# Optimization experiments

Measured on AMD Instinct MI355X. Metric: run time of the kernel, lower is better.

The kernel has to match this reference:

```python
import jax, jax.numpy as jnp
import numpy as np

B, H, E = 1024, 2048, 1024

def _xavier(key, shape):
    # torch xavier_normal_ on [1, out, in]: std = sqrt(2/(fan_in+fan_out)) over last two dims
    fan_out, fan_in = shape[-2], shape[-1]
    std = (2.0 / (fan_in + fan_out)) ** 0.5
    return jax.random.normal(key, shape, jnp.float32) * std

def setup_inputs() -> dict:
    key = jax.random.key(0)
    ks = jax.random.split(key, 17)
    inp = {
        'x': jax.random.normal(ks[0], (B, E, 1), jnp.float32),
        'c': jax.random.normal(ks[1], (B, H, 1), jnp.float32),
        'h': jax.random.normal(ks[2], (B, H, 1), jnp.float32),
        'W_xi': _xavier(ks[3], (1, H, E)), 'W_hi': _xavier(ks[4], (1, H, H)), 'B_i': _xavier(ks[5], (1, H, 1)),
        'W_xg': _xavier(ks[6], (1, H, E)), 'W_hg': _xavier(ks[7], (1, H, H)), 'B_g': _xavier(ks[8], (1, H, 1)),
        'W_xf': _xavier(ks[9], (1, H, E)), 'W_hf': _xavier(ks[10], (1, H, H)), 'B_f': _xavier(ks[11], (1, H, 1)),
        'W_xo': _xavier(ks[12], (1, H, E)), 'W_ho': _xavier(ks[13], (1, H, H)), 'B_o': _xavier(ks[14], (1, H, 1)),
        'W_hy': _xavier(ks[15], (1, E, H)), 'B_y': _xavier(ks[16], (1, E, 1)),
    }
    return inp

def reference(x, c, h, W_xi, W_hi, B_i, W_xg, W_hg, B_g, W_xf, W_hf, B_f, W_xo, W_ho, B_o, W_hy, B_y):
    # jnp.matmul broadcasts the leading batch dim: [1,H,E] @ [B,E,1] -> [B,H,1]
    i = jax.nn.sigmoid(jnp.matmul(W_xi, x) + jnp.matmul(W_hi, h) + B_i)
    g = jnp.tanh(jnp.matmul(W_xg, x) + jnp.matmul(W_hg, h) + B_g)
    f = jax.nn.sigmoid(jnp.matmul(W_xf, x) + jnp.matmul(W_hf, h) + B_f)
    c_new = f * c + i * g
    o = jax.nn.sigmoid(jnp.matmul(W_xo, x) + jnp.matmul(W_ho, h) + B_o)
    h_new = o * c_new  # NOTE: source uses o*c (no tanh), faithful to original
    y = jnp.tanh(jnp.matmul(W_hy, h_new) + B_y)
    return (y, c_new, h_new)
```

## Files before the change

kernel.cpp:

```cpp
#include <hip/hip_runtime.h>

#define B_SZ 1024
#define H_SZ 2048
#define E_SZ 1024

typedef float  f32x4 __attribute__((ext_vector_type(4)));
typedef short  s16x8 __attribute__((ext_vector_type(8)));

__device__ __forceinline__ unsigned short f2bf(float f) {
    unsigned u = __float_as_uint(f);
    u = u + 0x7fffu + ((u >> 16) & 1u);
    return (unsigned short)(u >> 16);
}
__device__ __forceinline__ float bf2f(unsigned short s) {
    return __uint_as_float(((unsigned)s) << 16);
}
__device__ __forceinline__ float sigm(float v) {
    return 1.0f / (1.0f + __expf(-v));
}
__device__ __forceinline__ unsigned cvtpk(float lo, float hi) {
    unsigned r;
    asm("v_cvt_pk_bf16_f32 %0, %1, %2" : "=v"(r) : "v"(lo), "v"(hi));
    return r;
}

__device__ __forceinline__ void gll(const unsigned short* g, unsigned short* l) {
    __builtin_amdgcn_global_load_lds(
        (const __attribute__((address_space(1))) unsigned int*)g,
        (__attribute__((address_space(3))) unsigned int*)l, 16, 0, 0);
}

struct CastArgs {
    const float*    src[10];
    unsigned short* dst[10];
    int             n[10];
};

__global__ __launch_bounds__(256) void cast_kernel(CastArgs a) {
    const int arr = blockIdx.y;
    const int n = a.n[arr];
    const float* __restrict__ s = a.src[arr];
    unsigned short* __restrict__ d = a.dst[arr];
    const int stride = gridDim.x * 256 * 4;
    for (int i = (blockIdx.x * 256 + threadIdx.x) * 4; i < n; i += stride) {
        float4 v = *(const float4*)(s + i);
        ushort4 o;
        o.x = f2bf(v.x); o.y = f2bf(v.y); o.z = f2bf(v.z); o.w = f2bf(v.w);
        *(ushort4*)(d + i) = o;
    }
}

__device__ __forceinline__ void gemm_gates4(
    const unsigned short* __restrict__ A,
    const unsigned short* __restrict__ W0,
    const unsigned short* __restrict__ W1,
    const unsigned short* __restrict__ W2,
    const unsigned short* __restrict__ W3,
    int ld, int kLen, int m0, int n0h,
    unsigned short* lA, unsigned short* lB,
    f32x4 acc[4][4], int t)
{
    const int lane = t & 63;
    const int w    = t >> 6;
    const int wr   = (w >> 1) << 6;
    const int wc   = (w & 1) << 6;
    const int lr   = lane & 15;
    const int q4   = lane >> 4;

    const int srow = t >> 3;
    const int scol = ((t & 7) ^ (srow & 7)) << 3;
    const unsigned short* gA = A + (size_t)(m0 + srow) * ld + scol;
    const size_t st32 = (size_t)32 * ld;
    const size_t boff = (size_t)(n0h + srow) * ld + scol;
    const unsigned short* gB0 = W0 + boff;
    const unsigned short* gB1 = W1 + boff;
    const unsigned short* gB2 = W2 + boff;
    const unsigned short* gB3 = W3 + boff;

    const int cb0 = ((q4    ) ^ (lr & 7)) << 3;
    const int cb1 = ((4 + q4) ^ (lr & 7)) << 3;

    for (int k0 = 0; k0 < kLen; k0 += 64) {
#pragma unroll
        for (int p = 0; p < 4; ++p)
            gll(gA + k0 + p * st32, lA + (t + 256 * p) * 8);
        gll(gB0 + k0, lB + t * 8);
        gll(gB1 + k0, lB + (t + 256) * 8);
        gll(gB2 + k0, lB + (t + 512) * 8);
        gll(gB3 + k0, lB + (t + 768) * 8);
        __syncthreads();

#pragma unroll
        for (int ks = 0; ks < 2; ++ks) {
            const int cb = ks ? cb1 : cb0;
            s16x8 af[4], bfr[4];
#pragma unroll
            for (int i = 0; i < 4; ++i)
                af[i] = *(const s16x8*)(lA + (wr + i * 16 + lr) * 64 + cb);
#pragma unroll
            for (int j = 0; j < 4; ++j)
                bfr[j] = *(const s16x8*)(lB + (wc + j * 16 + lr) * 64 + cb);
#pragma unroll
            for (int i = 0; i < 4; ++i)
#pragma unroll
                for (int j = 0; j < 4; ++j)
                    acc[i][j] = __builtin_amdgcn_mfma_f32_16x16x32_bf16(
                        af[i], bfr[j], acc[i][j], 0, 0, 0);
        }
        __syncthreads();
    }
}

struct GatesCellArgs {
    const unsigned short *Xb, *Hb, *Wxb, *Whb;
    const float *bias[4];
    const float *cin;
    float *c_out, *h_out;
    unsigned short *HnB;
};

__global__ __launch_bounds__(256, 2) void gates_cell_kernel(GatesCellArgs a) {
    __shared__ unsigned short smem[16384];
    unsigned short* lA = smem;
    unsigned short* lB = smem + 8192;

    const int t   = threadIdx.x;
    const int b   = blockIdx.x;
    const int xcd = b & 7;
    const int i_  = b >> 3;
    const int nt  = xcd * 8 + (i_ >> 3);
    const int m0  = (i_ & 7) * 128;
    const int n0h = nt * 32;

    const size_t HE = (size_t)H_SZ * E_SZ, HH = (size_t)H_SZ * H_SZ;

    f32x4 acc[4][4] = {};
    gemm_gates4(a.Xb, a.Wxb, a.Wxb + HE, a.Wxb + 2 * HE, a.Wxb + 3 * HE,
                E_SZ, E_SZ, m0, n0h, lA, lB, acc, t);
    gemm_gates4(a.Hb, a.Whb, a.Whb + HH, a.Whb + 2 * HH, a.Whb + 3 * HH,
                H_SZ, H_SZ, m0, n0h, lA, lB, acc, t);

    const int lane = t & 63, w = t >> 6;
    const int wr = (w >> 1) << 6, wc = (w & 1) << 6;
    const int lr = lane & 15, rq = (lane >> 4) << 2;
#pragma unroll
    for (int j = 0; j < 4; ++j) {
        const int col = wc + j * 16 + lr;
        const int q   = col >> 5;
        const float bv = a.bias[q][n0h + (col & 31)];
#pragma unroll
        for (int i = 0; i < 4; ++i) {
#pragma unroll
            for (int r = 0; r < 4; ++r) {
                const int row = wr + i * 16 + rq + r;
                const float v = acc[i][j][r] + bv;
                const float act = (q == 1) ? tanhf(v) : sigm(v);
                smem[row * 128 + col] = f2bf(act);
            }
        }
    }
    __syncthreads();

    {
        const int row = t >> 1;
        const int hc  = (t & 1) * 16;
        const unsigned short* ex = smem + row * 128;
        s16x8 i0 = *(const s16x8*)(ex + hc);
        s16x8 i1 = *(const s16x8*)(ex + hc + 8);
        s16x8 g0 = *(const s16x8*)(ex + 32 + hc);
        s16x8 g1 = *(const s16x8*)(ex + 32 + hc + 8);
        s16x8 fg0 = *(const s16x8*)(ex + 64 + hc);
        s16x8 fg1 = *(const s16x8*)(ex + 64 + hc + 8);
        s16x8 o0 = *(const s16x8*)(ex + 96 + hc);
        s16x8 o1 = *(const s16x8*)(ex + 96 + hc + 8);

        const size_t gidx = (size_t)(m0 + row) * H_SZ + n0h + hc;
        float cn[16], hn[16];
#pragma unroll
        for (int k = 0; k < 16; ++k) {
            const float iv = bf2f((unsigned short)((k < 8 ? i0[k] : i1[k - 8])));
            const float gv = bf2f((unsigned short)((k < 8 ? g0[k] : g1[k - 8])));
            const float fv = bf2f((unsigned short)((k < 8 ? fg0[k] : fg1[k - 8])));
            const float ov = bf2f((unsigned short)((k < 8 ? o0[k] : o1[k - 8])));
            const float cv = a.cin[gidx + k];
            cn[k] = fv * cv + iv * gv;
            hn[k] = ov * cn[k];
        }
#pragma unroll
        for (int k = 0; k < 16; k += 4) {
            *(float4*)(a.c_out + gidx + k) = make_float4(cn[k], cn[k+1], cn[k+2], cn[k+3]);
            *(float4*)(a.h_out + gidx + k) = make_float4(hn[k], hn[k+1], hn[k+2], hn[k+3]);
            ushort4 hb;
            hb.x = f2bf(hn[k]);     hb.y = f2bf(hn[k+1]);
            hb.z = f2bf(hn[k+2]);   hb.w = f2bf(hn[k+3]);
            *(ushort4*)(a.HnB + gidx + k) = hb;
        }
    }
}

__device__ __forceinline__ void gemm_bk128(
    const unsigned short* __restrict__ A,
    const float* __restrict__ W,
    int ld, int kLen, int m0, int n0,
    unsigned short* lA, unsigned short* lB,
    f32x4 acc[4][4], int t)
{
    const int lane = t & 63;
    const int w    = t >> 6;
    const int wr   = (w >> 1) << 6;
    const int wc   = (w & 1) << 6;
    const int lr   = lane & 15;
    const int q4   = lane >> 4;

    const int srow = t >> 4;
    const int sblk = ((t & 15) ^ srow) << 3;
    const unsigned short* gA = A + (size_t)(m0 + srow) * ld + sblk;
    const float*          gW = W + (size_t)(n0 + srow) * ld + sblk;
    const size_t st16 = (size_t)16 * ld;

    f32x4 f0[8], f1[8];
#pragma unroll
    for (int p = 0; p < 8; ++p) {
        const float* s = gW + p * st16;
        f0[p] = *(const f32x4*)(s);
        f1[p] = *(const f32x4*)(s + 4);
    }

    for (int k0 = 0; k0 < kLen; k0 += 128) {
#pragma unroll
        for (int p = 0; p < 8; ++p) {
            uint4 pk;
            pk.x = cvtpk(f0[p].x, f0[p].y);
            pk.y = cvtpk(f0[p].z, f0[p].w);
            pk.z = cvtpk(f1[p].x, f1[p].y);
            pk.w = cvtpk(f1[p].z, f1[p].w);
            *(uint4*)(lB + (t + 256 * p) * 8) = pk;
        }
#pragma unroll
        for (int p = 0; p < 8; ++p)
            gll(gA + k0 + p * st16, lA + (t + 256 * p) * 8);
        __syncthreads();

        if (k0 + 128 < kLen) {
#pragma unroll
            for (int p = 0; p < 8; ++p) {
                const float* s = gW + (k0 + 128) + p * st16;
                f0[p] = *(const f32x4*)(s);
                f1[p] = *(const f32x4*)(s + 4);
            }
        }

#pragma unroll
        for (int ks = 0; ks < 4; ++ks) {
            s16x8 af[4], bfr[4];
#pragma unroll
            for (int i = 0; i < 4; ++i) {
                const int ra = wr + i * 16 + lr;
                af[i] = *(const s16x8*)(lA + ra * 128 +
                         ((((ks << 2) + q4) ^ (ra & 15)) << 3));
            }
#pragma unroll
            for (int j = 0; j < 4; ++j) {
                const int rb = wc + j * 16 + lr;
                bfr[j] = *(const s16x8*)(lB + rb * 128 +
                          ((((ks << 2) + q4) ^ (rb & 15)) << 3));
            }
#pragma unroll
            for (int i = 0; i < 4; ++i)
#pragma unroll
                for (int j = 0; j < 4; ++j)
                    acc[i][j] = __builtin_amdgcn_mfma_f32_16x16x32_bf16(
                        af[i], bfr[j], acc[i][j], 0, 0, 0);
        }
        __syncthreads();
    }
}

__global__ __launch_bounds__(256, 2) void y_split_kernel(
    const unsigned short* __restrict__ Hn,
    const float* __restrict__ Wy,
    float* __restrict__ part)
{
    __shared__ unsigned short lA[128 * 128];
    __shared__ unsigned short lB[128 * 128];
    const int t   = threadIdx.x;
    const int b   = blockIdx.x;
    const int xcd = b & 7;
    const int i_  = b >> 3;
    const int ns  = xcd * 4 + (i_ >> 3);
    const int m0  = (i_ & 7) * 128;
    const int n0  = (ns >> 2) * 128;
    const int s   = ns & 3;

    f32x4 acc[4][4] = {};
    gemm_bk128(Hn + s * 512, Wy + s * 512, H_SZ, 512, m0, n0, lA, lB, acc, t);

    const int lane = t & 63, w = t >> 6;
    const int wr = (w >> 1) << 6, wc = (w & 1) << 6;
    const int lr = lane & 15, rq = (lane >> 4) << 2;
    float* P = part + (size_t)s * B_SZ * E_SZ;
#pragma unroll
    for (int i = 0; i < 4; ++i) {
#pragma unroll
        for (int j = 0; j < 4; ++j) {
            const int n = n0 + wc + j * 16 + lr;
#pragma unroll
            for (int r = 0; r < 4; ++r) {
                const int m = m0 + wr + i * 16 + rq + r;
                P[(size_t)m * E_SZ + n] = acc[i][j][r];
            }
        }
    }
}

__global__ __launch_bounds__(256) void y_reduce_kernel(
    const float* __restrict__ part, const float* __restrict__ by,
    float* __restrict__ yout)
{
    const size_t BE = (size_t)B_SZ * E_SZ;
    const int idx = (blockIdx.x * 256 + threadIdx.x) * 4;
    float4 a = *(const float4*)(part + idx);
    float4 b2 = *(const float4*)(part + BE + idx);
    float4 c2 = *(const float4*)(part + 2 * BE + idx);
    float4 d2 = *(const float4*)(part + 3 * BE + idx);
    const int col = idx & (E_SZ - 1);
    float4 bv = *(const float4*)(by + col);
    float4 o;
    o.x = tanhf(a.x + b2.x + c2.x + d2.x + bv.x);
    o.y = tanhf(a.y + b2.y + c2.y + d2.y + bv.y);
    o.z = tanhf(a.z + b2.z + c2.z + d2.z + bv.z);
    o.w = tanhf(a.w + b2.w + c2.w + d2.w + bv.w);
    *(float4*)(yout + idx) = o;
}

extern "C" void kernel_launch(void* const* d_in, const int* in_sizes, int n_in,
                              void* d_out, int out_size, void* d_ws, size_t ws_size,
                              hipStream_t stream) {
    const float* x   = (const float*)d_in[0];
    const float* c   = (const float*)d_in[1];
    const float* h   = (const float*)d_in[2];
    const float* Wxi = (const float*)d_in[3];
    const float* Whi = (const float*)d_in[4];
    const float* Bi  = (const float*)d_in[5];
    const float* Wxg = (const float*)d_in[6];
    const float* Whg = (const float*)d_in[7];
    const float* Bg  = (const float*)d_in[8];
    const float* Wxf = (const float*)d_in[9];
    const float* Whf = (const float*)d_in[10];
    const float* Bf  = (const float*)d_in[11];
    const float* Wxo = (const float*)d_in[12];
    const float* Who = (const float*)d_in[13];
    const float* Bo  = (const float*)d_in[14];
    const float* Why = (const float*)d_in[15];
    const float* By  = (const float*)d_in[16];

    const size_t BE = (size_t)B_SZ * E_SZ, BH = (size_t)B_SZ * H_SZ;
    const size_t HE = (size_t)H_SZ * E_SZ, HH = (size_t)H_SZ * H_SZ;

    unsigned short* ws  = (unsigned short*)d_ws;
    unsigned short* Xb  = ws;
    unsigned short* Hb  = Xb + BE;
    unsigned short* Wxb = Hb + BH;
    unsigned short* Whb = Wxb + 4 * HE;
    unsigned short* HnB = Whb + 4 * HH;
    float*          ypart = (float*)(HnB + BH);

    CastArgs ca;
    ca.src[0] = x;   ca.dst[0] = Xb;          ca.n[0] = (int)BE;
    ca.src[1] = h;   ca.dst[1] = Hb;          ca.n[1] = (int)BH;
    ca.src[2] = Wxi; ca.dst[2] = Wxb;         ca.n[2] = (int)HE;
    ca.src[3] = Wxg; ca.dst[3] = Wxb + HE;    ca.n[3] = (int)HE;
    ca.src[4] = Wxf; ca.dst[4] = Wxb + 2*HE;  ca.n[4] = (int)HE;
    ca.src[5] = Wxo; ca.dst[5] = Wxb + 3*HE;  ca.n[5] = (int)HE;
    ca.src[6] = Whi; ca.dst[6] = Whb;         ca.n[6] = (int)HH;
    ca.src[7] = Whg; ca.dst[7] = Whb + HH;    ca.n[7] = (int)HH;
    ca.src[8] = Whf; ca.dst[8] = Whb + 2*HH;  ca.n[8] = (int)HH;
    ca.src[9] = Who; ca.dst[9] = Whb + 3*HH;  ca.n[9] = (int)HH;
    hipLaunchKernelGGL(cast_kernel, dim3(512, 10), dim3(256), 0, stream, ca);

    float* y_out = (float*)d_out;
    float* c_out = y_out + BE;
    float* h_out = c_out + BH;

    GatesCellArgs ga;
    ga.Xb = Xb; ga.Hb = Hb; ga.Wxb = Wxb; ga.Whb = Whb;
    ga.bias[0] = Bi; ga.bias[1] = Bg; ga.bias[2] = Bf; ga.bias[3] = Bo;
    ga.cin = c; ga.c_out = c_out; ga.h_out = h_out; ga.HnB = HnB;
    hipLaunchKernelGGL(gates_cell_kernel, dim3(512), dim3(256), 0, stream, ga);

    hipLaunchKernelGGL(y_split_kernel, dim3(256), dim3(256), 0, stream,
                       HnB, Why, ypart);
    hipLaunchKernelGGL(y_reduce_kernel, dim3((unsigned)(BE / 1024)), dim3(256), 0, stream,
                       ypart, By, y_out);
}
```

Baseline: 262.4 us.

## Shrink gates tile to 64 rows, pre-cast W_hy, deepen y split-K

The gates kernel tile drops from 128 to 64 batch rows, doubling the grid to 1024 blocks and raising the occupancy target to 4 blocks per CU. W_hy is now cast to bf16 in the shared cast kernel, so the y GEMM uses global_load_lds for both operands instead of converting fp32 in registers. The y GEMM split-K goes from 4 to 8 slices with a 512-block grid, and its partials reuse the Wxb workspace region. The cost is more weight reloads per output in the gates GEMM, an extra cast pass over W_hy, and twice as many partials to read in the reduction.

After: 266.8 us. No clear change (+1.7%).

```diff
diff --git a/kernel.cpp b/kernel.cpp
--- a/kernel.cpp
+++ b/kernel.cpp
@@ -18,11 +18,6 @@
 __device__ __forceinline__ float sigm(float v) {
     return 1.0f / (1.0f + __expf(-v));
 }
-__device__ __forceinline__ unsigned cvtpk(float lo, float hi) {
-    unsigned r;
-    asm("v_cvt_pk_bf16_f32 %0, %1, %2" : "=v"(r) : "v"(lo), "v"(hi));
-    return r;
-}
 
 __device__ __forceinline__ void gll(const unsigned short* g, unsigned short* l) {
     __builtin_amdgcn_global_load_lds(
@@ -31,9 +26,9 @@
 }
 
 struct CastArgs {
-    const float*    src[10];
-    unsigned short* dst[10];
-    int             n[10];
+    const float*    src[11];
+    unsigned short* dst[11];
+    int             n[11];
 };
 
 __global__ __launch_bounds__(256) void cast_kernel(CastArgs a) {
@@ -50,7 +45,7 @@
     }
 }
 
-__device__ __forceinline__ void gemm_gates4(
+__device__ __forceinline__ void gemm_gates4_m64(
     const unsigned short* __restrict__ A,
     const unsigned short* __restrict__ W0,
     const unsigned short* __restrict__ W1,
@@ -58,11 +53,11 @@
     const unsigned short* __restrict__ W3,
     int ld, int kLen, int m0, int n0h,
     unsigned short* lA, unsigned short* lB,
-    f32x4 acc[4][4], int t)
+    f32x4 acc[2][4], int t)
 {
     const int lane = t & 63;
     const int w    = t >> 6;
-    const int wr   = (w >> 1) << 6;
+    const int wr   = (w >> 1) << 5;
     const int wc   = (w & 1) << 6;
     const int lr   = lane & 15;
     const int q4   = lane >> 4;
@@ -81,9 +76,8 @@
     const int cb1 = ((4 + q4) ^ (lr & 7)) << 3;
 
     for (int k0 = 0; k0 < kLen; k0 += 64) {
-#pragma unroll
-        for (int p = 0; p < 4; ++p)
-            gll(gA + k0 + p * st32, lA + (t + 256 * p) * 8);
+        gll(gA + k0,        lA + t * 8);
+        gll(gA + k0 + st32, lA + (t + 256) * 8);
         gll(gB0 + k0, lB + t * 8);
         gll(gB1 + k0, lB + (t + 256) * 8);
         gll(gB2 + k0, lB + (t + 512) * 8);
@@ -93,15 +87,15 @@
 #pragma unroll
         for (int ks = 0; ks < 2; ++ks) {
             const int cb = ks ? cb1 : cb0;
-            s16x8 af[4], bfr[4];
-#pragma unroll
-            for (int i = 0; i < 4; ++i)
+            s16x8 af[2], bfr[4];
+#pragma unroll
+            for (int i = 0; i < 2; ++i)
                 af[i] = *(const s16x8*)(lA + (wr + i * 16 + lr) * 64 + cb);
 #pragma unroll
             for (int j = 0; j < 4; ++j)
                 bfr[j] = *(const s16x8*)(lB + (wc + j * 16 + lr) * 64 + cb);
 #pragma unroll
-            for (int i = 0; i < 4; ++i)
+            for (int i = 0; i < 2; ++i)
 #pragma unroll
                 for (int j = 0; j < 4; ++j)
                     acc[i][j] = __builtin_amdgcn_mfma_f32_16x16x32_bf16(
@@ -119,29 +113,29 @@
     unsigned short *HnB;
 };
 
-__global__ __launch_bounds__(256, 2) void gates_cell_kernel(GatesCellArgs a) {
-    __shared__ unsigned short smem[16384];
+__global__ __launch_bounds__(256, 4) void gates_cell_kernel(GatesCellArgs a) {
+    __shared__ unsigned short smem[12288];
     unsigned short* lA = smem;
-    unsigned short* lB = smem + 8192;
+    unsigned short* lB = smem + 4096;
 
     const int t   = threadIdx.x;
     const int b   = blockIdx.x;
     const int xcd = b & 7;
     const int i_  = b >> 3;
-    const int nt  = xcd * 8 + (i_ >> 3);
-    const int m0  = (i_ & 7) * 128;
+    const int nt  = xcd * 8 + (i_ >> 4);
+    const int m0  = (i_ & 15) * 64;
     const int n0h = nt * 32;
 
     const size_t HE = (size_t)H_SZ * E_SZ, HH = (size_t)H_SZ * H_SZ;
 
-    f32x4 acc[4][4] = {};
-    gemm_gates4(a.Xb, a.Wxb, a.Wxb + HE, a.Wxb + 2 * HE, a.Wxb + 3 * HE,
-                E_SZ, E_SZ, m0, n0h, lA, lB, acc, t);
-    gemm_gates4(a.Hb, a.Whb, a.Whb + HH, a.Whb + 2 * HH, a.Whb + 3 * HH,
-                H_SZ, H_SZ, m0, n0h, lA, lB, acc, t);
+    f32x4 acc[2][4] = {};
+    gemm_gates4_m64(a.Xb, a.Wxb, a.Wxb + HE, a.Wxb + 2 * HE, a.Wxb + 3 * HE,
+                    E_SZ, E_SZ, m0, n0h, lA, lB, acc, t);
+    gemm_gates4_m64(a.Hb, a.Whb, a.Whb + HH, a.Whb + 2 * HH, a.Whb + 3 * HH,
+                    H_SZ, H_SZ, m0, n0h, lA, lB, acc, t);
 
     const int lane = t & 63, w = t >> 6;
-    const int wr = (w >> 1) << 6, wc = (w & 1) << 6;
+    const int wr = (w >> 1) << 5, wc = (w & 1) << 6;
     const int lr = lane & 15, rq = (lane >> 4) << 2;
 #pragma unroll
     for (int j = 0; j < 4; ++j) {
@@ -149,7 +143,7 @@
         const int q   = col >> 5;
         const float bv = a.bias[q][n0h + (col & 31)];
 #pragma unroll
-        for (int i = 0; i < 4; ++i) {
+        for (int i = 0; i < 2; ++i) {
 #pragma unroll
             for (int r = 0; r < 4; ++r) {
                 const int row = wr + i * 16 + rq + r;
@@ -162,32 +156,28 @@
     __syncthreads();
 
     {
-        const int row = t >> 1;
-        const int hc  = (t & 1) * 16;
+        const int row = t >> 2;
+        const int hc  = (t & 3) * 8;
         const unsigned short* ex = smem + row * 128;
-        s16x8 i0 = *(const s16x8*)(ex + hc);
-        s16x8 i1 = *(const s16x8*)(ex + hc + 8);
-        s16x8 g0 = *(const s16x8*)(ex + 32 + hc);
-        s16x8 g1 = *(const s16x8*)(ex + 32 + hc + 8);
-        s16x8 fg0 = *(const s16x8*)(ex + 64 + hc);
-        s16x8 fg1 = *(const s16x8*)(ex + 64 + hc + 8);
-        s16x8 o0 = *(const s16x8*)(ex + 96 + hc);
-        s16x8 o1 = *(const s16x8*)(ex + 96 + hc + 8);
+        s16x8 iv8 = *(const s16x8*)(ex + hc);
+        s16x8 gv8 = *(const s16x8*)(ex + 32 + hc);
+        s16x8 fv8 = *(const s16x8*)(ex + 64 + hc);
+        s16x8 ov8 = *(const s16x8*)(ex + 96 + hc);
 
         const size_t gidx = (size_t)(m0 + row) * H_SZ + n0h + hc;
-        float cn[16], hn[16];
-#pragma unroll
-        for (int k = 0; k < 16; ++k) {
-            const float iv = bf2f((unsigned short)((k < 8 ? i0[k] : i1[k - 8])));
-            const float gv = bf2f((unsigned short)((k < 8 ? g0[k] : g1[k - 8])));
-            const float fv = bf2f((unsigned short)((k < 8 ? fg0[k] : fg1[k - 8])));
-            const float ov = bf2f((unsigned short)((k < 8 ? o0[k] : o1[k - 8])));
+        float cn[8], hn[8];
+#pragma unroll
+        for (int k = 0; k < 8; ++k) {
+            const float iv = bf2f((unsigned short)iv8[k]);
+            const float gv = bf2f((unsigned short)gv8[k]);
+            const float fv = bf2f((unsigned short)fv8[k]);
+            const float ov = bf2f((unsigned short)ov8[k]);
             const float cv = a.cin[gidx + k];
             cn[k] = fv * cv + iv * gv;
             hn[k] = ov * cn[k];
         }
 #pragma unroll
-        for (int k = 0; k < 16; k += 4) {
+        for (int k = 0; k < 8; k += 4) {
             *(float4*)(a.c_out + gidx + k) = make_float4(cn[k], cn[k+1], cn[k+2], cn[k+3]);
             *(float4*)(a.h_out + gidx + k) = make_float4(hn[k], hn[k+1], hn[k+2], hn[k+3]);
             ushort4 hb;
@@ -198,9 +188,9 @@
     }
 }
 
-__device__ __forceinline__ void gemm_bk128(
+__device__ __forceinline__ void gemm_accum64(
     const unsigned short* __restrict__ A,
-    const float* __restrict__ W,
+    const unsigned short* __restrict__ W,
     int ld, int kLen, int m0, int n0,
     unsigned short* lA, unsigned short* lB,
     f32x4 acc[4][4], int t)
@@ -212,59 +202,34 @@
     const int lr   = lane & 15;
     const int q4   = lane >> 4;
 
-    const int srow = t >> 4;
-    const int sblk = ((t & 15) ^ srow) << 3;
-    const unsigned short* gA = A + (size_t)(m0 + srow) * ld + sblk;
-    const float*          gW = W + (size_t)(n0 + srow) * ld + sblk;
-    const size_t st16 = (size_t)16 * ld;
-
-    f32x4 f0[8], f1[8];
-#pragma unroll
-    for (int p = 0; p < 8; ++p) {
-        const float* s = gW + p * st16;
-        f0[p] = *(const f32x4*)(s);
-        f1[p] = *(const f32x4*)(s + 4);
-    }
-
-    for (int k0 = 0; k0 < kLen; k0 += 128) {
-#pragma unroll
-        for (int p = 0; p < 8; ++p) {
-            uint4 pk;
-            pk.x = cvtpk(f0[p].x, f0[p].y);
-            pk.y = cvtpk(f0[p].z, f0[p].w);
-            pk.z = cvtpk(f1[p].x, f1[p].y);
-            pk.w = cvtpk(f1[p].z, f1[p].w);
-            *(uint4*)(lB + (t + 256 * p) * 8) = pk;
-        }
-#pragma unroll
-        for (int p = 0; p < 8; ++p)
-            gll(gA + k0 + p * st16, lA + (t + 256 * p) * 8);
+    const int srow = t >> 3;
+    const int scol = ((t & 7) ^ (srow & 7)) << 3;
+    const unsigned short* gA = A + (size_t)(m0 + srow) * ld + scol;
+    const unsigned short* gB = W + (size_t)(n0 + srow) * ld + scol;
+    const size_t st32 = (size_t)32 * ld;
+
+    const int cb0 = ((q4    ) ^ (lr & 7)) << 3;
+    const int cb1 = ((4 + q4) ^ (lr & 7)) << 3;
+
+    for (int k0 = 0; k0 < kLen; k0 += 64) {
+#pragma unroll
+        for (int p = 0; p < 4; ++p)
+            gll(gA + k0 + p * st32, lA + (t + 256 * p) * 8);
+#pragma unroll
+        for (int p = 0; p < 4; ++p)
+            gll(gB + k0 + p * st32, lB + (t + 256 * p) * 8);
         __syncthreads();
 
-        if (k0 + 128 < kLen) {
-#pragma unroll
-            for (int p = 0; p < 8; ++p) {
-                const float* s = gW + (k0 + 128) + p * st16;
-                f0[p] = *(const f32x4*)(s);
-                f1[p] = *(const f32x4*)(s + 4);
-            }
-        }
-
-#pragma unroll
-        for (int ks = 0; ks < 4; ++ks) {
+#pragma unroll
+        for (int ks = 0; ks < 2; ++ks) {
+            const int cb = ks ? cb1 : cb0;
             s16x8 af[4], bfr[4];
 #pragma unroll
-            for (int i = 0; i < 4; ++i) {
-                const int ra = wr + i * 16 + lr;
-                af[i] = *(const s16x8*)(lA + ra * 128 +
-                         ((((ks << 2) + q4) ^ (ra & 15)) << 3));
-            }
-#pragma unroll
-            for (int j = 0; j < 4; ++j) {
-                const int rb = wc + j * 16 + lr;
-                bfr[j] = *(const s16x8*)(lB + rb * 128 +
-                          ((((ks << 2) + q4) ^ (rb & 15)) << 3));
-            }
+            for (int i = 0; i < 4; ++i)
+                af[i] = *(const s16x8*)(lA + (wr + i * 16 + lr) * 64 + cb);
+#pragma unroll
+            for (int j = 0; j < 4; ++j)
+                bfr[j] = *(const s16x8*)(lB + (wc + j * 16 + lr) * 64 + cb);
 #pragma unroll
             for (int i = 0; i < 4; ++i)
 #pragma unroll
@@ -278,22 +243,22 @@
 
 __global__ __launch_bounds__(256, 2) void y_split_kernel(
     const unsigned short* __restrict__ Hn,
-    const float* __restrict__ Wy,
+    const unsigned short* __restrict__ Wy,
     float* __restrict__ part)
 {
-    __shared__ unsigned short lA[128 * 128];
-    __shared__ unsigned short lB[128 * 128];
+    __shared__ unsigned short lA[128 * 64];
+    __shared__ unsigned short lB[128 * 64];
     const int t   = threadIdx.x;
     const int b   = blockIdx.x;
     const int xcd = b & 7;
     const int i_  = b >> 3;
-    const int ns  = xcd * 4 + (i_ >> 3);
+    const int ns  = xcd * 8 + (i_ >> 3);
     const int m0  = (i_ & 7) * 128;
-    const int n0  = (ns >> 2) * 128;
-    const int s   = ns & 3;
+    const int n0  = (ns >> 3) * 128;
+    const int s   = ns & 7;
 
     f32x4 acc[4][4] = {};
-    gemm_bk128(Hn + s * 512, Wy + s * 512, H_SZ, 512, m0, n0, lA, lB, acc, t);
+    gemm_accum64(Hn + s * 256, Wy + s * 256, H_SZ, 256, m0, n0, lA, lB, acc, t);
 
     const int lane = t & 63, w = t >> 6;
     const int wr = (w >> 1) << 6, wc = (w & 1) << 6;
@@ -319,17 +284,19 @@
 {
     const size_t BE = (size_t)B_SZ * E_SZ;
     const int idx = (blockIdx.x * 256 + threadIdx.x) * 4;
-    float4 a = *(const float4*)(part + idx);
-    float4 b2 = *(const float4*)(part + BE + idx);
-    float4 c2 = *(const float4*)(part + 2 * BE + idx);
-    float4 d2 = *(const float4*)(part + 3 * BE + idx);
+    float4 s0 = *(const float4*)(part + idx);
+#pragma unroll
+    for (int s = 1; s < 8; ++s) {
+        float4 p = *(const float4*)(part + (size_t)s * BE + idx);
+        s0.x += p.x; s0.y += p.y; s0.z += p.z; s0.w += p.w;
+    }
     const int col = idx & (E_SZ - 1);
     float4 bv = *(const float4*)(by + col);
     float4 o;
-    o.x = tanhf(a.x + b2.x + c2.x + d2.x + bv.x);
-    o.y = tanhf(a.y + b2.y + c2.y + d2.y + bv.y);
-    o.z = tanhf(a.z + b2.z + c2.z + d2.z + bv.z);
-    o.w = tanhf(a.w + b2.w + c2.w + d2.w + bv.w);
+    o.x = tanhf(s0.x + bv.x);
+    o.y = tanhf(s0.y + bv.y);
+    o.z = tanhf(s0.z + bv.z);
+    o.w = tanhf(s0.w + bv.w);
     *(float4*)(yout + idx) = o;
 }
 
@@ -356,27 +323,30 @@
 
     const size_t BE = (size_t)B_SZ * E_SZ, BH = (size_t)B_SZ * H_SZ;
     const size_t HE = (size_t)H_SZ * E_SZ, HH = (size_t)H_SZ * H_SZ;
-
-    unsigned short* ws  = (unsigned short*)d_ws;
-    unsigned short* Xb  = ws;
-    unsigned short* Hb  = Xb + BE;
-    unsigned short* Wxb = Hb + BH;
-    unsigned short* Whb = Wxb + 4 * HE;
-    unsigned short* HnB = Whb + 4 * HH;
-    float*          ypart = (float*)(HnB + BH);
+    const size_t EH = (size_t)E_SZ * H_SZ;
+
+    unsigned short* ws   = (unsigned short*)d_ws;
+    unsigned short* Xb   = ws;
+    unsigned short* Hb   = Xb + BE;
+    unsigned short* Wxb  = Hb + BH;
+    unsigned short* Whb  = Wxb + 4 * HE;
+    unsigned short* Whyb = Whb + 4 * HH;
+    unsigned short* HnB  = Whyb + EH;
+    float*          ypart = (float*)Wxb;
 
     CastArgs ca;
-    ca.src[0] = x;   ca.dst[0] = Xb;          ca.n[0] = (int)BE;
-    ca.src[1] = h;   ca.dst[1] = Hb;          ca.n[1] = (int)BH;
-    ca.src[2] = Wxi; ca.dst[2] = Wxb;         ca.n[2] = (int)HE;
-    ca.src[3] = Wxg; ca.dst[3] = Wxb + HE;    ca.n[3] = (int)HE;
-    ca.src[4] = Wxf; ca.dst[4] = Wxb + 2*HE;  ca.n[4] = (int)HE;
-    ca.src[5] = Wxo; ca.dst[5] = Wxb + 3*HE;  ca.n[5] = (int)HE;
-    ca.src[6] = Whi; ca.dst[6] = Whb;         ca.n[6] = (int)HH;
-    ca.src[7] = Whg; ca.dst[7] = Whb + HH;    ca.n[7] = (int)HH;
-    ca.src[8] = Whf; ca.dst[8] = Whb + 2*HH;  ca.n[8] = (int)HH;
-    ca.src[9] = Who; ca.dst[9] = Whb + 3*HH;  ca.n[9] = (int)HH;
-    hipLaunchKernelGGL(cast_kernel, dim3(512, 10), dim3(256), 0, stream, ca);
+    ca.src[0]  = x;   ca.dst[0]  = Xb;          ca.n[0]  = (int)BE;
+    ca.src[1]  = h;   ca.dst[1]  = Hb;          ca.n[1]  = (int)BH;
+    ca.src[2]  = Wxi; ca.dst[2]  = Wxb;         ca.n[2]  = (int)HE;
+    ca.src[3]  = Wxg; ca.dst[3]  = Wxb + HE;    ca.n[3]  = (int)HE;
+    ca.src[4]  = Wxf; ca.dst[4]  = Wxb + 2*HE;  ca.n[4]  = (int)HE;
+    ca.src[5]  = Wxo; ca.dst[5]  = Wxb + 3*HE;  ca.n[5]  = (int)HE;
+    ca.src[6]  = Whi; ca.dst[6]  = Whb;         ca.n[6]  = (int)HH;
+    ca.src[7]  = Whg; ca.dst[7]  = Whb + HH;    ca.n[7]  = (int)HH;
+    ca.src[8]  = Whf; ca.dst[8]  = Whb + 2*HH;  ca.n[8]  = (int)HH;
+    ca.src[9]  = Who; ca.dst[9]  = Whb + 3*HH;  ca.n[9]  = (int)HH;
+    ca.src[10] = Why; ca.dst[10] = Whyb;        ca.n[10] = (int)EH;
+    hipLaunchKernelGGL(cast_kernel, dim3(512, 11), dim3(256), 0, stream, ca);
 
     float* y_out = (float*)d_out;
     float* c_out = y_out + BE;
@@ -386,10 +356,10 @@
     ga.Xb = Xb; ga.Hb = Hb; ga.Wxb = Wxb; ga.Whb = Whb;
     ga.bias[0] = Bi; ga.bias[1] = Bg; ga.bias[2] = Bf; ga.bias[3] = Bo;
     ga.cin = c; ga.c_out = c_out; ga.h_out = h_out; ga.HnB = HnB;
-    hipLaunchKernelGGL(gates_cell_kernel, dim3(512), dim3(256), 0, stream, ga);
-
-    hipLaunchKernelGGL(y_split_kernel, dim3(256), dim3(256), 0, stream,
-                       HnB, Why, ypart);
+    hipLaunchKernelGGL(gates_cell_kernel, dim3(1024), dim3(256), 0, stream, ga);
+
+    hipLaunchKernelGGL(y_split_kernel, dim3(512), dim3(256), 0, stream,
+                       HnB, Whyb, ypart);
     hipLaunchKernelGGL(y_reduce_kernel, dim3((unsigned)(BE / 1024)), dim3(256), 0, stream,
                        ypart, By, y_out);
 }
```

## Restructure gates GEMM into 4-slot software-pipelined 256-row tiles with 512 threads

Applied to the files above, without the earlier changes.

The gates kernel now uses 512-thread blocks that each cover 256 batch rows instead of 128, which halves the grid and doubles reuse of each weight tile. The K loop is split into half-tiles staged through a 4-slot LDS ring with explicit vmcnt waits, raw barriers and setprio around the MFMA bursts, so global loads overlap compute. The epilogue LDS stride is padded to 136 to avoid bank conflicts, and ypart is aliased onto the bf16 Wx workspace, which is dead by the time it is written. In exchange the kernel uses more LDS per block and depends on hand-tuned wait counts, which is fragile.

Result: slower. 320.6 us (+22.2%).

```diff
diff --git a/kernel.cpp b/kernel.cpp
--- a/kernel.cpp
+++ b/kernel.cpp
@@ -50,67 +50,6 @@
     }
 }
 
-__device__ __forceinline__ void gemm_gates4(
-    const unsigned short* __restrict__ A,
-    const unsigned short* __restrict__ W0,
-    const unsigned short* __restrict__ W1,
-    const unsigned short* __restrict__ W2,
-    const unsigned short* __restrict__ W3,
-    int ld, int kLen, int m0, int n0h,
-    unsigned short* lA, unsigned short* lB,
-    f32x4 acc[4][4], int t)
-{
-    const int lane = t & 63;
-    const int w    = t >> 6;
-    const int wr   = (w >> 1) << 6;
-    const int wc   = (w & 1) << 6;
-    const int lr   = lane & 15;
-    const int q4   = lane >> 4;
-
-    const int srow = t >> 3;
-    const int scol = ((t & 7) ^ (srow & 7)) << 3;
-    const unsigned short* gA = A + (size_t)(m0 + srow) * ld + scol;
-    const size_t st32 = (size_t)32 * ld;
-    const size_t boff = (size_t)(n0h + srow) * ld + scol;
-    const unsigned short* gB0 = W0 + boff;
-    const unsigned short* gB1 = W1 + boff;
-    const unsigned short* gB2 = W2 + boff;
-    const unsigned short* gB3 = W3 + boff;
-
-    const int cb0 = ((q4    ) ^ (lr & 7)) << 3;
-    const int cb1 = ((4 + q4) ^ (lr & 7)) << 3;
-
-    for (int k0 = 0; k0 < kLen; k0 += 64) {
-#pragma unroll
-        for (int p = 0; p < 4; ++p)
-            gll(gA + k0 + p * st32, lA + (t + 256 * p) * 8);
-        gll(gB0 + k0, lB + t * 8);
-        gll(gB1 + k0, lB + (t + 256) * 8);
-        gll(gB2 + k0, lB + (t + 512) * 8);
-        gll(gB3 + k0, lB + (t + 768) * 8);
-        __syncthreads();
-
-#pragma unroll
-        for (int ks = 0; ks < 2; ++ks) {
-            const int cb = ks ? cb1 : cb0;
-            s16x8 af[4], bfr[4];
-#pragma unroll
-            for (int i = 0; i < 4; ++i)
-                af[i] = *(const s16x8*)(lA + (wr + i * 16 + lr) * 64 + cb);
-#pragma unroll
-            for (int j = 0; j < 4; ++j)
-                bfr[j] = *(const s16x8*)(lB + (wc + j * 16 + lr) * 64 + cb);
-#pragma unroll
-            for (int i = 0; i < 4; ++i)
-#pragma unroll
-                for (int j = 0; j < 4; ++j)
-                    acc[i][j] = __builtin_amdgcn_mfma_f32_16x16x32_bf16(
-                        af[i], bfr[j], acc[i][j], 0, 0, 0);
-        }
-        __syncthreads();
-    }
-}
-
 struct GatesCellArgs {
     const unsigned short *Xb, *Hb, *Wxb, *Whb;
     const float *bias[4];
@@ -119,43 +58,123 @@
     unsigned short *HnB;
 };
 
-__global__ __launch_bounds__(256, 2) void gates_cell_kernel(GatesCellArgs a) {
-    __shared__ unsigned short smem[16384];
+__global__ __launch_bounds__(512, 2) void gates_cell_kernel(GatesCellArgs a) {
+    __shared__ unsigned short smem[49152];
     unsigned short* lA = smem;
-    unsigned short* lB = smem + 8192;
+    unsigned short* lB = smem + 32768;
 
     const int t   = threadIdx.x;
     const int b   = blockIdx.x;
     const int xcd = b & 7;
     const int i_  = b >> 3;
-    const int nt  = xcd * 8 + (i_ >> 3);
-    const int m0  = (i_ & 7) * 128;
+    const int nt  = xcd * 8 + (i_ >> 2);
+    const int m0  = (i_ & 3) * 256;
     const int n0h = nt * 32;
 
     const size_t HE = (size_t)H_SZ * E_SZ, HH = (size_t)H_SZ * H_SZ;
 
+    const int rA  = t >> 2;
+    const int swz = (((t & 3) ^ ((t >> 3) & 3)) << 3);
+    const unsigned short* xa  = a.Xb + (size_t)(m0 + rA) * E_SZ + swz;
+    const unsigned short* xa2 = xa + (size_t)128 * E_SZ;
+    const unsigned short* ha  = a.Hb + (size_t)(m0 + rA) * H_SZ + swz;
+    const unsigned short* ha2 = ha + (size_t)128 * H_SZ;
+    const int g    = t >> 7;
+    const int rowB = (t >> 2) & 31;
+    const unsigned short* wxSel = a.Wxb + (size_t)g * HE
+                                + (size_t)(n0h + rowB) * E_SZ + swz;
+    const unsigned short* whSel = a.Whb + (size_t)g * HH
+                                + (size_t)(n0h + rowB) * H_SZ + swz;
+
+    auto stage = [&](int kt, int kh, int slot) {
+        unsigned short* dA = lA + slot * 8192 + t * 8;
+        unsigned short* dB = lB + slot * 4096 + t * 8;
+        if (kt < 16) {
+            const int k = kt * 64 + kh * 32;
+            gll(xa + k, dA); gll(xa2 + k, dA + 4096); gll(wxSel + k, dB);
+        } else {
+            const int k = (kt - 16) * 64 + kh * 32;
+            gll(ha + k, dA); gll(ha2 + k, dA + 4096); gll(whSel + k, dB);
+        }
+    };
+
+    const int lane = t & 63;
+    const int w    = t >> 6;
+    const int wr   = (w >> 1) << 6;
+    const int wc   = (w & 1) << 6;
+    const int lr   = lane & 15;
+    const int q4   = lane >> 4;
+    int offA[4], offB[4];
+#pragma unroll
+    for (int i = 0; i < 4; ++i) {
+        const int ra = wr + i * 16 + lr;
+        offA[i] = ra * 32 + ((q4 ^ ((ra >> 1) & 3)) << 3);
+        const int rb = wc + i * 16 + lr;
+        offB[i] = rb * 32 + ((q4 ^ ((rb >> 1) & 3)) << 3);
+    }
+
     f32x4 acc[4][4] = {};
-    gemm_gates4(a.Xb, a.Wxb, a.Wxb + HE, a.Wxb + 2 * HE, a.Wxb + 3 * HE,
-                E_SZ, E_SZ, m0, n0h, lA, lB, acc, t);
-    gemm_gates4(a.Hb, a.Whb, a.Whb + HH, a.Whb + 2 * HH, a.Whb + 3 * HH,
-                H_SZ, H_SZ, m0, n0h, lA, lB, acc, t);
-
-    const int lane = t & 63, w = t >> 6;
-    const int wr = (w >> 1) << 6, wc = (w & 1) << 6;
-    const int lr = lane & 15, rq = (lane >> 4) << 2;
+
+    stage(0, 0, 0); stage(0, 1, 1); stage(1, 0, 2);
+    asm volatile("s_waitcnt vmcnt(6)" ::: "memory");
+    __builtin_amdgcn_s_barrier();
+
+#define PHASE(SLOT, STAGE_STMT, VMC)                                      \
+  {                                                                       \
+    const unsigned short* pA = lA + (SLOT) * 8192;                        \
+    const unsigned short* pB = lB + (SLOT) * 4096;                        \
+    s16x8 af[4], bv[4];                                                   \
+    af[0] = *(const s16x8*)(pA + offA[0]);                                \
+    af[1] = *(const s16x8*)(pA + offA[1]);                                \
+    af[2] = *(const s16x8*)(pA + offA[2]);                                \
+    af[3] = *(const s16x8*)(pA + offA[3]);                                \
+    bv[0] = *(const s16x8*)(pB + offB[0]);                                \
+    bv[1] = *(const s16x8*)(pB + offB[1]);                                \
+    bv[2] = *(const s16x8*)(pB + offB[2]);                                \
+    bv[3] = *(const s16x8*)(pB + offB[3]);                                \
+    STAGE_STMT;                                                           \
+    asm volatile("s_waitcnt vmcnt(" VMC ")" ::: "memory");                \
+    __builtin_amdgcn_s_barrier();                                         \
+    asm volatile("s_waitcnt lgkmcnt(0)" ::: "memory");                    \
+    __builtin_amdgcn_sched_barrier(0);                                    \
+    __builtin_amdgcn_s_setprio(1);                                        \
+    _Pragma("unroll") for (int i2 = 0; i2 < 4; ++i2)                      \
+      _Pragma("unroll") for (int j2 = 0; j2 < 4; ++j2)                    \
+        acc[i2][j2] = __builtin_amdgcn_mfma_f32_16x16x32_bf16(            \
+            af[i2], bv[j2], acc[i2][j2], 0, 0, 0);                        \
+    __builtin_amdgcn_s_setprio(0);                                        \
+  }
+
+#pragma unroll 1
+    for (int mt = 0; mt < 23; ++mt) {
+        const int kt = mt * 2;
+        PHASE(0, stage(kt + 1, 1, 3), "6");
+        PHASE(1, stage(kt + 2, 0, 0), "6");
+        PHASE(2, stage(kt + 2, 1, 1), "6");
+        PHASE(3, stage(kt + 3, 0, 2), "6");
+    }
+    PHASE(0, stage(47, 1, 3), "6");
+    PHASE(1, , "3");
+    PHASE(2, , "0");
+    PHASE(3, , "0");
+#undef PHASE
+
+    __syncthreads();
+
+    const int rq = (lane >> 4) << 2;
 #pragma unroll
     for (int j = 0; j < 4; ++j) {
         const int col = wc + j * 16 + lr;
         const int q   = col >> 5;
-        const float bv = a.bias[q][n0h + (col & 31)];
+        const float bvv = a.bias[q][n0h + (col & 31)];
 #pragma unroll
         for (int i = 0; i < 4; ++i) {
 #pragma unroll
             for (int r = 0; r < 4; ++r) {
                 const int row = wr + i * 16 + rq + r;
-                const float v = acc[i][j][r] + bv;
+                const float v = acc[i][j][r] + bvv;
                 const float act = (q == 1) ? tanhf(v) : sigm(v);
-                smem[row * 128 + col] = f2bf(act);
+                smem[row * 136 + col] = f2bf(act);
             }
         }
     }
@@ -163,25 +182,25 @@
 
     {
         const int row = t >> 1;
-        const int hc  = (t & 1) * 16;
-        const unsigned short* ex = smem + row * 128;
-        s16x8 i0 = *(const s16x8*)(ex + hc);
-        s16x8 i1 = *(const s16x8*)(ex + hc + 8);
-        s16x8 g0 = *(const s16x8*)(ex + 32 + hc);
-        s16x8 g1 = *(const s16x8*)(ex + 32 + hc + 8);
-        s16x8 fg0 = *(const s16x8*)(ex + 64 + hc);
-        s16x8 fg1 = *(const s16x8*)(ex + 64 + hc + 8);
-        s16x8 o0 = *(const s16x8*)(ex + 96 + hc);
-        s16x8 o1 = *(const s16x8*)(ex + 96 + hc + 8);
-
-        const size_t gidx = (size_t)(m0 + row) * H_SZ + n0h + hc;
+        const int hl0 = (t & 1) * 16;
+        const unsigned short* ex = smem + row * 136;
+        s16x8 i0 = *(const s16x8*)(ex + hl0);
+        s16x8 i1 = *(const s16x8*)(ex + hl0 + 8);
+        s16x8 g0 = *(const s16x8*)(ex + 32 + hl0);
+        s16x8 g1 = *(const s16x8*)(ex + 32 + hl0 + 8);
+        s16x8 f0 = *(const s16x8*)(ex + 64 + hl0);
+        s16x8 f1 = *(const s16x8*)(ex + 64 + hl0 + 8);
+        s16x8 o0 = *(const s16x8*)(ex + 96 + hl0);
+        s16x8 o1 = *(const s16x8*)(ex + 96 + hl0 + 8);
+
+        const size_t gidx = (size_t)(m0 + row) * H_SZ + n0h + hl0;
         float cn[16], hn[16];
 #pragma unroll
         for (int k = 0; k < 16; ++k) {
-            const float iv = bf2f((unsigned short)((k < 8 ? i0[k] : i1[k - 8])));
-            const float gv = bf2f((unsigned short)((k < 8 ? g0[k] : g1[k - 8])));
-            const float fv = bf2f((unsigned short)((k < 8 ? fg0[k] : fg1[k - 8])));
-            const float ov = bf2f((unsigned short)((k < 8 ? o0[k] : o1[k - 8])));
+            const float iv = bf2f((unsigned short)(k < 8 ? i0[k] : i1[k - 8]));
+            const float gv = bf2f((unsigned short)(k < 8 ? g0[k] : g1[k - 8]));
+            const float fv = bf2f((unsigned short)(k < 8 ? f0[k] : f1[k - 8]));
+            const float ov = bf2f((unsigned short)(k < 8 ? o0[k] : o1[k - 8]));
             const float cv = a.cin[gidx + k];
             cn[k] = fv * cv + iv * gv;
             hn[k] = ov * cn[k];
@@ -191,8 +210,8 @@
             *(float4*)(a.c_out + gidx + k) = make_float4(cn[k], cn[k+1], cn[k+2], cn[k+3]);
             *(float4*)(a.h_out + gidx + k) = make_float4(hn[k], hn[k+1], hn[k+2], hn[k+3]);
             ushort4 hb;
-            hb.x = f2bf(hn[k]);     hb.y = f2bf(hn[k+1]);
-            hb.z = f2bf(hn[k+2]);   hb.w = f2bf(hn[k+3]);
+            hb.x = f2bf(hn[k]);   hb.y = f2bf(hn[k+1]);
+            hb.z = f2bf(hn[k+2]); hb.w = f2bf(hn[k+3]);
             *(ushort4*)(a.HnB + gidx + k) = hb;
         }
     }
@@ -363,7 +382,7 @@
     unsigned short* Wxb = Hb + BH;
     unsigned short* Whb = Wxb + 4 * HE;
     unsigned short* HnB = Whb + 4 * HH;
-    float*          ypart = (float*)(HnB + BH);
+    float*          ypart = (float*)Wxb;
 
     CastArgs ca;
     ca.src[0] = x;   ca.dst[0] = Xb;          ca.n[0] = (int)BE;
@@ -386,7 +405,7 @@
     ga.Xb = Xb; ga.Hb = Hb; ga.Wxb = Wxb; ga.Whb = Whb;
     ga.bias[0] = Bi; ga.bias[1] = Bg; ga.bias[2] = Bf; ga.bias[3] = Bo;
     ga.cin = c; ga.c_out = c_out; ga.h_out = h_out; ga.HnB = HnB;
-    hipLaunchKernelGGL(gates_cell_kernel, dim3(512), dim3(256), 0, stream, ga);
+    hipLaunchKernelGGL(gates_cell_kernel, dim3(256), dim3(512), 0, stream, ga);
 
     hipLaunchKernelGGL(y_split_kernel, dim3(256), dim3(256), 0, stream,
                        HnB, Why, ypart);
```

## Double-buffer LDS in fused gates GEMM to overlap global loads with MFMA

Applied to the files above, without the earlier changes.

Replaces the two sequential single-buffered K loops (x-part then h-part) in the gates kernel with one merged 48-step loop over two LDS buffers. The next tile's direct-to-LDS loads are issued before computing the current one, with an explicit vmcnt wait and raw barriers. The epilogue staging stride is padded from 128 to 136 to reduce LDS bank conflicts. LDS use doubles to 64 KB per block, which may limit the two-blocks-per-CU occupancy target.

Result: slower. 326.7 us (+24.5%).

```diff
diff --git a/kernel.cpp b/kernel.cpp
--- a/kernel.cpp
+++ b/kernel.cpp
@@ -50,67 +50,6 @@
     }
 }
 
-__device__ __forceinline__ void gemm_gates4(
-    const unsigned short* __restrict__ A,
-    const unsigned short* __restrict__ W0,
-    const unsigned short* __restrict__ W1,
-    const unsigned short* __restrict__ W2,
-    const unsigned short* __restrict__ W3,
-    int ld, int kLen, int m0, int n0h,
-    unsigned short* lA, unsigned short* lB,
-    f32x4 acc[4][4], int t)
-{
-    const int lane = t & 63;
-    const int w    = t >> 6;
-    const int wr   = (w >> 1) << 6;
-    const int wc   = (w & 1) << 6;
-    const int lr   = lane & 15;
-    const int q4   = lane >> 4;
-
-    const int srow = t >> 3;
-    const int scol = ((t & 7) ^ (srow & 7)) << 3;
-    const unsigned short* gA = A + (size_t)(m0 + srow) * ld + scol;
-    const size_t st32 = (size_t)32 * ld;
-    const size_t boff = (size_t)(n0h + srow) * ld + scol;
-    const unsigned short* gB0 = W0 + boff;
-    const unsigned short* gB1 = W1 + boff;
-    const unsigned short* gB2 = W2 + boff;
-    const unsigned short* gB3 = W3 + boff;
-
-    const int cb0 = ((q4    ) ^ (lr & 7)) << 3;
-    const int cb1 = ((4 + q4) ^ (lr & 7)) << 3;
-
-    for (int k0 = 0; k0 < kLen; k0 += 64) {
-#pragma unroll
-        for (int p = 0; p < 4; ++p)
-            gll(gA + k0 + p * st32, lA + (t + 256 * p) * 8);
-        gll(gB0 + k0, lB + t * 8);
-        gll(gB1 + k0, lB + (t + 256) * 8);
-        gll(gB2 + k0, lB + (t + 512) * 8);
-        gll(gB3 + k0, lB + (t + 768) * 8);
-        __syncthreads();
-
-#pragma unroll
-        for (int ks = 0; ks < 2; ++ks) {
-            const int cb = ks ? cb1 : cb0;
-            s16x8 af[4], bfr[4];
-#pragma unroll
-            for (int i = 0; i < 4; ++i)
-                af[i] = *(const s16x8*)(lA + (wr + i * 16 + lr) * 64 + cb);
-#pragma unroll
-            for (int j = 0; j < 4; ++j)
-                bfr[j] = *(const s16x8*)(lB + (wc + j * 16 + lr) * 64 + cb);
-#pragma unroll
-            for (int i = 0; i < 4; ++i)
-#pragma unroll
-                for (int j = 0; j < 4; ++j)
-                    acc[i][j] = __builtin_amdgcn_mfma_f32_16x16x32_bf16(
-                        af[i], bfr[j], acc[i][j], 0, 0, 0);
-        }
-        __syncthreads();
-    }
-}
-
 struct GatesCellArgs {
     const unsigned short *Xb, *Hb, *Wxb, *Whb;
     const float *bias[4];
@@ -120,9 +59,9 @@
 };
 
 __global__ __launch_bounds__(256, 2) void gates_cell_kernel(GatesCellArgs a) {
-    __shared__ unsigned short smem[16384];
+    __shared__ unsigned short smem[32768];
     unsigned short* lA = smem;
-    unsigned short* lB = smem + 8192;
+    unsigned short* lB = smem + 16384;
 
     const int t   = threadIdx.x;
     const int b   = blockIdx.x;
@@ -134,15 +73,89 @@
 
     const size_t HE = (size_t)H_SZ * E_SZ, HH = (size_t)H_SZ * H_SZ;
 
-    f32x4 acc[4][4] = {};
-    gemm_gates4(a.Xb, a.Wxb, a.Wxb + HE, a.Wxb + 2 * HE, a.Wxb + 3 * HE,
-                E_SZ, E_SZ, m0, n0h, lA, lB, acc, t);
-    gemm_gates4(a.Hb, a.Whb, a.Whb + HH, a.Whb + 2 * HH, a.Whb + 3 * HH,
-                H_SZ, H_SZ, m0, n0h, lA, lB, acc, t);
+    const int srow = t >> 3;
+    const int scol = ((t & 7) ^ (srow & 7)) << 3;
+    const unsigned short* xaE = a.Xb + (size_t)(m0 + srow) * E_SZ + scol;
+    const unsigned short* xaH = a.Hb + (size_t)(m0 + srow) * H_SZ + scol;
+    const size_t stE = (size_t)32 * E_SZ, stH = (size_t)32 * H_SZ;
+    const size_t bE  = (size_t)(n0h + srow) * E_SZ + scol;
+    const size_t bH  = (size_t)(n0h + srow) * H_SZ + scol;
+    const unsigned short* wE0 = a.Wxb + bE;
+    const unsigned short* wE1 = a.Wxb + HE + bE;
+    const unsigned short* wE2 = a.Wxb + 2 * HE + bE;
+    const unsigned short* wE3 = a.Wxb + 3 * HE + bE;
+    const unsigned short* wH0 = a.Whb + bH;
+    const unsigned short* wH1 = a.Whb + HH + bH;
+    const unsigned short* wH2 = a.Whb + 2 * HH + bH;
+    const unsigned short* wH3 = a.Whb + 3 * HH + bH;
+
+    auto stage = [&](int kk, int buf) {
+        unsigned short* dA = lA + buf * 8192 + t * 8;
+        unsigned short* dB = lB + buf * 8192 + t * 8;
+        if (kk < 16) {
+            const int k = kk * 64;
+            gll(xaE + k,           dA);
+            gll(xaE + k + stE,     dA + 2048);
+            gll(xaE + k + 2 * stE, dA + 4096);
+            gll(xaE + k + 3 * stE, dA + 6144);
+            gll(wE0 + k, dB);        gll(wE1 + k, dB + 2048);
+            gll(wE2 + k, dB + 4096); gll(wE3 + k, dB + 6144);
+        } else {
+            const int k = (kk - 16) * 64;
+            gll(xaH + k,           dA);
+            gll(xaH + k + stH,     dA + 2048);
+            gll(xaH + k + 2 * stH, dA + 4096);
+            gll(xaH + k + 3 * stH, dA + 6144);
+            gll(wH0 + k, dB);        gll(wH1 + k, dB + 2048);
+            gll(wH2 + k, dB + 4096); gll(wH3 + k, dB + 6144);
+        }
+    };
 
     const int lane = t & 63, w = t >> 6;
     const int wr = (w >> 1) << 6, wc = (w & 1) << 6;
-    const int lr = lane & 15, rq = (lane >> 4) << 2;
+    const int lr = lane & 15, q4 = lane >> 4;
+    const int cb0 = ((q4    ) ^ (lr & 7)) << 3;
+    const int cb1 = ((4 + q4) ^ (lr & 7)) << 3;
+
+    f32x4 acc[4][4] = {};
+
+    auto compute = [&](int buf) {
+        const unsigned short* pA = lA + buf * 8192;
+        const unsigned short* pB = lB + buf * 8192;
+#pragma unroll
+        for (int ks = 0; ks < 2; ++ks) {
+            const int cb = ks ? cb1 : cb0;
+            s16x8 af[4], bfr[4];
+#pragma unroll
+            for (int i = 0; i < 4; ++i)
+                af[i] = *(const s16x8*)(pA + (wr + i * 16 + lr) * 64 + cb);
+#pragma unroll
+            for (int j = 0; j < 4; ++j)
+                bfr[j] = *(const s16x8*)(pB + (wc + j * 16 + lr) * 64 + cb);
+#pragma unroll
+            for (int i = 0; i < 4; ++i)
+#pragma unroll
+                for (int j = 0; j < 4; ++j)
+                    acc[i][j] = __builtin_amdgcn_mfma_f32_16x16x32_bf16(
+                        af[i], bfr[j], acc[i][j], 0, 0, 0);
+        }
+    };
+
+    stage(0, 0);
+#pragma unroll 1
+    for (int kk = 0; kk < 47; ++kk) {
+        stage(kk + 1, (kk + 1) & 1);
+        asm volatile("s_waitcnt vmcnt(8)" ::: "memory");
+        asm volatile("s_barrier" ::: "memory");
+        compute(kk & 1);
+        asm volatile("s_barrier" ::: "memory");
+    }
+    asm volatile("s_waitcnt vmcnt(0)" ::: "memory");
+    asm volatile("s_barrier" ::: "memory");
+    compute(1);
+    __syncthreads();
+
+    const int rq = (lane >> 4) << 2;
 #pragma unroll
     for (int j = 0; j < 4; ++j) {
         const int col = wc + j * 16 + lr;
@@ -155,7 +168,7 @@
                 const int row = wr + i * 16 + rq + r;
                 const float v = acc[i][j][r] + bv;
                 const float act = (q == 1) ? tanhf(v) : sigm(v);
-                smem[row * 128 + col] = f2bf(act);
+                smem[row * 136 + col] = f2bf(act);
             }
         }
     }
@@ -163,25 +176,25 @@
 
     {
         const int row = t >> 1;
-        const int hc  = (t & 1) * 16;
-        const unsigned short* ex = smem + row * 128;
-        s16x8 i0 = *(const s16x8*)(ex + hc);
-        s16x8 i1 = *(const s16x8*)(ex + hc + 8);
-        s16x8 g0 = *(const s16x8*)(ex + 32 + hc);
-        s16x8 g1 = *(const s16x8*)(ex + 32 + hc + 8);
-        s16x8 fg0 = *(const s16x8*)(ex + 64 + hc);
-        s16x8 fg1 = *(const s16x8*)(ex + 64 + hc + 8);
-        s16x8 o0 = *(const s16x8*)(ex + 96 + hc);
-        s16x8 o1 = *(const s16x8*)(ex + 96 + hc + 8);
-
-        const size_t gidx = (size_t)(m0 + row) * H_SZ + n0h + hc;
+        const int hl0 = (t & 1) * 16;
+        const unsigned short* ex = smem + row * 136;
+        s16x8 i0 = *(const s16x8*)(ex + hl0);
+        s16x8 i1 = *(const s16x8*)(ex + hl0 + 8);
+        s16x8 g0 = *(const s16x8*)(ex + 32 + hl0);
+        s16x8 g1 = *(const s16x8*)(ex + 32 + hl0 + 8);
+        s16x8 f0 = *(const s16x8*)(ex + 64 + hl0);
+        s16x8 f1 = *(const s16x8*)(ex + 64 + hl0 + 8);
+        s16x8 o0 = *(const s16x8*)(ex + 96 + hl0);
+        s16x8 o1 = *(const s16x8*)(ex + 96 + hl0 + 8);
+
+        const size_t gidx = (size_t)(m0 + row) * H_SZ + n0h + hl0;
         float cn[16], hn[16];
 #pragma unroll
         for (int k = 0; k < 16; ++k) {
-            const float iv = bf2f((unsigned short)((k < 8 ? i0[k] : i1[k - 8])));
-            const float gv = bf2f((unsigned short)((k < 8 ? g0[k] : g1[k - 8])));
-            const float fv = bf2f((unsigned short)((k < 8 ? fg0[k] : fg1[k - 8])));
-            const float ov = bf2f((unsigned short)((k < 8 ? o0[k] : o1[k - 8])));
+            const float iv = bf2f((unsigned short)(k < 8 ? i0[k] : i1[k - 8]));
+            const float gv = bf2f((unsigned short)(k < 8 ? g0[k] : g1[k - 8]));
+            const float fv = bf2f((unsigned short)(k < 8 ? f0[k] : f1[k - 8]));
+            const float ov = bf2f((unsigned short)(k < 8 ? o0[k] : o1[k - 8]));
             const float cv = a.cin[gidx + k];
             cn[k] = fv * cv + iv * gv;
             hn[k] = ov * cn[k];
@@ -191,8 +204,8 @@
             *(float4*)(a.c_out + gidx + k) = make_float4(cn[k], cn[k+1], cn[k+2], cn[k+3]);
             *(float4*)(a.h_out + gidx + k) = make_float4(hn[k], hn[k+1], hn[k+2], hn[k+3]);
             ushort4 hb;
-            hb.x = f2bf(hn[k]);     hb.y = f2bf(hn[k+1]);
-            hb.z = f2bf(hn[k+2]);   hb.w = f2bf(hn[k+3]);
+            hb.x = f2bf(hn[k]);   hb.y = f2bf(hn[k+1]);
+            hb.z = f2bf(hn[k+2]); hb.w = f2bf(hn[k+3]);
             *(ushort4*)(a.HnB + gidx + k) = hb;
         }
     }
```
